# Optimization experiments

Hardware: AMD Instinct MI355X
Metric: run time of the kernel (lower is better)

The kernel has to match this reference:

```python
import jax, jax.numpy as jnp
import numpy as np

N_NODES = 500000
N_EDGES = 1250000
N_FEAT = 128
HIDDEN = 64
N_CLASSES = 10
N_GRAPHS = 512


def setup_inputs() -> dict:
    key = jax.random.key(0)
    ks = jax.random.split(key, 12)
    x = jax.random.normal(ks[0], (N_NODES, N_FEAT), dtype=jnp.float32)
    edge_index = jax.random.randint(ks[1], (2, N_EDGES), 0, N_NODES, dtype=jnp.int64)
    batch_index = jnp.sort(jax.random.randint(ks[2], (N_NODES,), 0, N_GRAPHS, dtype=jnp.int64))
    def glorot(k, fan_in, fan_out):
        s = jnp.sqrt(6.0 / (fan_in + fan_out))
        return jax.random.uniform(k, (fan_in, fan_out), jnp.float32, -s, s)
    return {
        "x": x,
        "edge_index": edge_index,
        "batch_index": batch_index,
        "W0": glorot(ks[3], N_FEAT, HIDDEN),
        "b0": jnp.zeros((HIDDEN,), jnp.float32),
        "W1": glorot(ks[4], HIDDEN, HIDDEN),
        "b1": jnp.zeros((HIDDEN,), jnp.float32),
        "W2": glorot(ks[5], HIDDEN, HIDDEN),
        "b2": jnp.zeros((HIDDEN,), jnp.float32),
        "Wout": glorot(ks[6], 2 * HIDDEN, N_CLASSES),
        "bout": jnp.zeros((N_CLASSES,), jnp.float32),
    }


def _gcn_norm(edge_index, n_nodes):
    # PyG GCNConv default: add self-loops, symmetric D^-1/2 (A+I) D^-1/2 norm.
    loop = jnp.arange(n_nodes, dtype=edge_index.dtype)
    src = jnp.concatenate([edge_index[0], loop])  # message sources
    dst = jnp.concatenate([edge_index[1], loop])  # aggregation targets
    deg = jax.ops.segment_sum(jnp.ones_like(dst, dtype=jnp.float32), dst,
                              num_segments=n_nodes)
    dinv = jnp.where(deg > 0, jax.lax.rsqrt(deg), 0.0)
    norm = dinv[src] * dinv[dst]  # [E+N]
    return src, dst, norm


def _gcn_conv(h, W, b, src, dst, norm, n_nodes):
    h = h @ W  # transform first (PyG applies lin before propagate)
    msg = h[src] * norm[:, None]  # gather + scale, [E+N, C]
    out = jax.ops.segment_sum(msg, dst, num_segments=n_nodes)
    return out + b


def reference(x, edge_index, batch_index, W0, b0, W1, b1, W2, b2, Wout, bout):
    n = x.shape[0]
    src, dst, norm = _gcn_norm(edge_index, n)
    h = jax.nn.relu(_gcn_conv(x, W0, b0, src, dst, norm, n))
    h = jax.nn.relu(_gcn_conv(h, W1, b1, src, dst, norm, n))
    h = jax.nn.relu(_gcn_conv(h, W2, b2, src, dst, norm, n))
    # global mean / max pool over graphs
    gsum = jax.ops.segment_sum(h, batch_index, num_segments=N_GRAPHS)
    cnt = jax.ops.segment_sum(jnp.ones((n,), jnp.float32), batch_index,
                              num_segments=N_GRAPHS)
    gmean = gsum / jnp.maximum(cnt, 1.0)[:, None]
    gmax = jax.ops.segment_max(h, batch_index, num_segments=N_GRAPHS)
    gmax = jnp.where(jnp.isneginf(gmax), 0.0, gmax)  # guard empty graphs
    pooled = jnp.concatenate([gmean, gmax], axis=1)  # [G, 2H]
    return pooled @ Wout + bout
```

## Files before the change

kernel.cpp:

```cpp
#include <hip/hip_runtime.h>
#include <hip/hip_bf16.h>

#define NN 500000
#define NE 1250000
#define NF 128
#define NH 64
#define NC 10
#define NG 512
#define ELLW 8

typedef __attribute__((ext_vector_type(8))) short short8;
typedef __attribute__((ext_vector_type(4))) float floatx4;

__device__ __forceinline__ unsigned short f2bf(float f) {
  unsigned u = __builtin_bit_cast(unsigned, f);
  u += 0x7FFFu + ((u >> 16) & 1u);
  return (unsigned short)(u >> 16);
}
__device__ __forceinline__ float bf2f(unsigned short u) {
  return __builtin_bit_cast(float, (unsigned)u << 16);
}
__device__ __forceinline__ float asf(int i) { return __builtin_bit_cast(float, i); }

__global__ __launch_bounds__(256) void k_init(int* __restrict__ deg, int* __restrict__ cur,
                                              int* __restrict__ counter,
                                              float* __restrict__ gsum, int* __restrict__ gmax,
                                              int* __restrict__ gcnt,
                                              int4* __restrict__ ell4,
                                              const float* __restrict__ W0,
                                              const float* __restrict__ W1,
                                              const float* __restrict__ W2,
                                              unsigned short* __restrict__ Wt0,
                                              unsigned short* __restrict__ Wt1,
                                              unsigned short* __restrict__ Wt2) {
  int i = blockIdx.x * 256 + threadIdx.x;
  if (i < NN) {
    deg[i] = 0; cur[i] = 0;
    int4 p; p.x = i; p.y = 0; p.z = i; p.w = 0;
    ell4[(size_t)i * 4 + 0] = p;
    ell4[(size_t)i * 4 + 1] = p;
    ell4[(size_t)i * 4 + 2] = p;
    ell4[(size_t)i * 4 + 3] = p;
  }
  if (i == 0) *counter = 0;
  if (i < NG * 64) { gsum[i] = 0.f; gmax[i] = 0; }
  if (i < NG) gcnt[i] = 0;
  if (i < NF * 64) { int k = i / 64, n = i % 64; Wt0[n * NF + k] = f2bf(W0[i]); }
  if (i < 64 * 64) {
    int k = i / 64, n = i % 64;
    Wt1[n * 64 + k] = f2bf(W1[i]);
    Wt2[n * 64 + k] = f2bf(W2[i]);
  }
}

__global__ __launch_bounds__(256) void k_deg(const int* __restrict__ dst, int* __restrict__ deg) {
  int e = blockIdx.x * 256 + threadIdx.x;
  if (e < NE) atomicAdd(&deg[dst[e]], 1);
}

__global__ __launch_bounds__(256) void k_dinv(const int* __restrict__ deg,
                                              float* __restrict__ dinv,
                                              int* __restrict__ odeg) {
  int i = blockIdx.x * 256 + threadIdx.x;
  if (i < NN) {
    int d = deg[i];
    dinv[i] = rsqrtf((float)(d + 1));
    odeg[i] = d > ELLW ? d - ELLW : 0;
  }
}

__global__ __launch_bounds__(256) void k_rowstart(const int* __restrict__ deg,
                                                  int* __restrict__ row_start,
                                                  int* __restrict__ counter) {
  int i = blockIdx.x * 256 + threadIdx.x;
  int lane = threadIdx.x & 63;
  int d = (i < NN) ? deg[i] : 0;
  int incl = d;
#pragma unroll
  for (int off = 1; off < 64; off <<= 1) {
    int n = __shfl_up(incl, off, 64);
    if (lane >= off) incl += n;
  }
  int total = __shfl(incl, 63, 64);
  int base = 0;
  if (lane == 63) base = atomicAdd(counter, total);
  base = __shfl(base, 63, 64);
  if (i < NN) row_start[i] = base + incl - d;
}

__global__ __launch_bounds__(256) void k_fill(const int* __restrict__ ei,
                                              const float* __restrict__ dinv,
                                              int* __restrict__ cur,
                                              int2* __restrict__ ell,
                                              const int* __restrict__ ostart,
                                              int2* __restrict__ ovf) {
  int e = blockIdx.x * 256 + threadIdx.x;
  if (e >= NE) return;
  int s = ei[e];
  int d = ei[NE + e];
  float nrm = dinv[s] * dinv[d];
  int slot = atomicAdd(&cur[d], 1);
  int2 v;
  v.x = s;
  v.y = __builtin_bit_cast(int, nrm);
  if (slot < ELLW) ell[(size_t)d * ELLW + slot] = v;
  else ovf[ostart[d] + slot - ELLW] = v;
}

__global__ __launch_bounds__(256) void k_gemm_f32(const float* __restrict__ Ain,
                                                  const unsigned short* __restrict__ Wt,
                                                  unsigned short* __restrict__ linbf) {
  constexpr int K = 128, KC = 4, SP = K + 8;
  __shared__ unsigned short Wl[64 * SP];
  int tid = threadIdx.x;
  for (int idx = tid * 8; idx < 64 * K; idx += 2048) {
    int n = idx / K, k = idx % K;
    *(short8*)&Wl[n * SP + k] = *(const short8*)&Wt[idx];
  }
  __syncthreads();

  int lane = tid & 63, wave = tid >> 6;
  int quad = lane >> 4, l16 = lane & 15;

  short8 bfrag[4][KC];
#pragma unroll
  for (int nt = 0; nt < 4; ++nt)
#pragma unroll
    for (int kc = 0; kc < KC; ++kc)
      bfrag[nt][kc] = *(const short8*)&Wl[(nt * 16 + l16) * SP + kc * 32 + quad * 8];

  const int ntiles = NN / 16;
  for (int t0 = (blockIdx.x * 4 + wave) * 2; t0 < ntiles; t0 += gridDim.x * 8) {
    floatx4 acc[2][4];
    floatx4 araw[2][KC][2];
#pragma unroll
    for (int tt = 0; tt < 2; ++tt) {
      int arow = (t0 + tt) * 16 + l16;
      const float* Ab = Ain + (size_t)arow * K + quad * 8;
#pragma unroll
      for (int kc = 0; kc < KC; ++kc) {
        araw[tt][kc][0] = *(const floatx4*)(Ab + kc * 32);
        araw[tt][kc][1] = *(const floatx4*)(Ab + kc * 32 + 4);
      }
    }
#pragma unroll
    for (int tt = 0; tt < 2; ++tt) {
      floatx4 z = {0.f, 0.f, 0.f, 0.f};
#pragma unroll
      for (int nt = 0; nt < 4; ++nt) acc[tt][nt] = z;
#pragma unroll
      for (int kc = 0; kc < KC; ++kc) {
        short8 af;
#pragma unroll
        for (int q = 0; q < 4; ++q) {
          af[q] = (short)f2bf(araw[tt][kc][0][q]);
          af[q + 4] = (short)f2bf(araw[tt][kc][1][q]);
        }
#pragma unroll
        for (int nt = 0; nt < 4; ++nt)
          acc[tt][nt] = __builtin_amdgcn_mfma_f32_16x16x32_bf16(af, bfrag[nt][kc], acc[tt][nt], 0, 0, 0);
      }
#pragma unroll
      for (int i = 0; i < 4; ++i) {
        int r = (t0 + tt) * 16 + quad * 4 + i;
        unsigned short* lp = linbf + (size_t)r * 64 + l16;
#pragma unroll
        for (int nt = 0; nt < 4; ++nt) lp[nt * 16] = f2bf(acc[tt][nt][i]);
      }
    }
  }
}

__global__ __launch_bounds__(256) void k_agg(const unsigned short* __restrict__ linbf,
                                             const float* __restrict__ dinv,
                                             const float* __restrict__ bias,
                                             const int* __restrict__ deg,
                                             const int2* __restrict__ ell,
                                             const int* __restrict__ ostart,
                                             const int2* __restrict__ ovf,
                                             unsigned short* __restrict__ hout) {
  int r = blockIdx.x * 4 + (threadIdx.x >> 6);
  if (r >= NN) return;
  int c = threadIdx.x & 63;
  const int4* ellv = (const int4*)(ell + (size_t)r * ELLW);
  int4 q0 = ellv[0], q1 = ellv[1], q2 = ellv[2], q3 = ellv[3];
  int dg = deg[r];
  float dv = dinv[r];
  float bc = bias[c];
  float acc = bf2f(linbf[(size_t)r * 64 + c]) * dv * dv;

  acc = fmaf(asf(q0.y), bf2f(linbf[(size_t)q0.x * 64 + c]), acc);
  acc = fmaf(asf(q0.w), bf2f(linbf[(size_t)q0.z * 64 + c]), acc);
  acc = fmaf(asf(q1.y), bf2f(linbf[(size_t)q1.x * 64 + c]), acc);
  acc = fmaf(asf(q1.w), bf2f(linbf[(size_t)q1.z * 64 + c]), acc);
  if (dg > 4) {
    acc = fmaf(asf(q2.y), bf2f(linbf[(size_t)q2.x * 64 + c]), acc);
    acc = fmaf(asf(q2.w), bf2f(linbf[(size_t)q2.z * 64 + c]), acc);
    acc = fmaf(asf(q3.y), bf2f(linbf[(size_t)q3.x * 64 + c]), acc);
    acc = fmaf(asf(q3.w), bf2f(linbf[(size_t)q3.z * 64 + c]), acc);
  }
  if (dg > ELLW) {
    int rs = ostart[r];
    int on = dg - ELLW;
    for (int j = 0; j < on; j += 4) {
      int2 e0 = ovf[rs + j];
      int2 e1 = ovf[rs + j + 1];
      int2 e2 = ovf[rs + j + 2];
      int2 e3 = ovf[rs + j + 3];
      int rem = on - j;
      float n0 = asf(e0.y);
      float n1 = rem > 1 ? asf(e1.y) : 0.f;
      float n2 = rem > 2 ? asf(e2.y) : 0.f;
      float n3 = rem > 3 ? asf(e3.y) : 0.f;
      int s0 = e0.x;
      int s1 = rem > 1 ? e1.x : r;
      int s2 = rem > 2 ? e2.x : r;
      int s3 = rem > 3 ? e3.x : r;
      acc = fmaf(n0, bf2f(linbf[(size_t)s0 * 64 + c]), acc);
      acc = fmaf(n1, bf2f(linbf[(size_t)s1 * 64 + c]), acc);
      acc = fmaf(n2, bf2f(linbf[(size_t)s2 * 64 + c]), acc);
      acc = fmaf(n3, bf2f(linbf[(size_t)s3 * 64 + c]), acc);
    }
  }
  hout[(size_t)r * 64 + c] = f2bf(fmaxf(acc + bc, 0.f));
}

template <int POOL>
__global__ __launch_bounds__(256) void k_layer(const unsigned short* __restrict__ hin,
                                               const float* __restrict__ dinv,
                                               const float* __restrict__ bias,
                                               const int* __restrict__ deg,
                                               const int2* __restrict__ ell,
                                               const int* __restrict__ ostart,
                                               const int2* __restrict__ ovf,
                                               const unsigned short* __restrict__ Wt,
                                               unsigned short* __restrict__ hout,
                                               float* __restrict__ gsum,
                                               int* __restrict__ gmax,
                                               int* __restrict__ gcnt,
                                               const int* __restrict__ batch) {
  constexpr int SP = 72;
  constexpr int SLDS = POOL ? (64 * 66 * 2) : (64 * SP);
  __shared__ unsigned short Sl[SLDS];
  float* smemf = (float*)Sl;
  int tid = threadIdx.x;
  int lane = tid & 63, wave = tid >> 6, quad = lane >> 4, l16 = lane & 15;

  for (int idx = tid * 8; idx < 64 * 64; idx += 2048)
    *(short8*)&Sl[idx] = *(const short8*)&Wt[idx];
  __syncthreads();
  short8 bfrag[4][2];
#pragma unroll
  for (int nt = 0; nt < 4; ++nt)
#pragma unroll
    for (int kc = 0; kc < 2; ++kc)
      bfrag[nt][kc] = *(const short8*)&Sl[(nt * 16 + l16) * 64 + kc * 32 + quad * 8];
  float bb[4];
#pragma unroll
  for (int nt = 0; nt < 4; ++nt) bb[nt] = bias[nt * 16 + l16];
  __syncthreads();

  int base = blockIdx.x * 64;
  int rbase = base + wave * 16;

#pragma unroll 4
  for (int j = 0; j < 16; ++j) {
    int r = rbase + j;
    float acc = 0.f;
    if (r < NN) {
      const int4* ellv = (const int4*)(ell + (size_t)r * ELLW);
      int4 q0 = ellv[0], q1 = ellv[1], q2 = ellv[2], q3 = ellv[3];
      int dg = deg[r];
      float dv = dinv[r];
      acc = bf2f(hin[(size_t)r * 64 + lane]) * dv * dv;
      acc = fmaf(asf(q0.y), bf2f(hin[(size_t)q0.x * 64 + lane]), acc);
      acc = fmaf(asf(q0.w), bf2f(hin[(size_t)q0.z * 64 + lane]), acc);
      acc = fmaf(asf(q1.y), bf2f(hin[(size_t)q1.x * 64 + lane]), acc);
      acc = fmaf(asf(q1.w), bf2f(hin[(size_t)q1.z * 64 + lane]), acc);
      if (dg > 4) {
        acc = fmaf(asf(q2.y), bf2f(hin[(size_t)q2.x * 64 + lane]), acc);
        acc = fmaf(asf(q2.w), bf2f(hin[(size_t)q2.z * 64 + lane]), acc);
        acc = fmaf(asf(q3.y), bf2f(hin[(size_t)q3.x * 64 + lane]), acc);
        acc = fmaf(asf(q3.w), bf2f(hin[(size_t)q3.z * 64 + lane]), acc);
      }
      if (dg > ELLW) {
        int rs = ostart[r];
        int on = dg - ELLW;
        for (int jj = 0; jj < on; jj += 4) {
          int2 e0 = ovf[rs + jj];
          int2 e1 = ovf[rs + jj + 1];
          int2 e2 = ovf[rs + jj + 2];
          int2 e3 = ovf[rs + jj + 3];
          int rem = on - jj;
          float n0 = asf(e0.y);
          float n1 = rem > 1 ? asf(e1.y) : 0.f;
          float n2 = rem > 2 ? asf(e2.y) : 0.f;
          float n3 = rem > 3 ? asf(e3.y) : 0.f;
          int s0 = e0.x;
          int s1 = rem > 1 ? e1.x : r;
          int s2 = rem > 2 ? e2.x : r;
          int s3 = rem > 3 ? e3.x : r;
          acc = fmaf(n0, bf2f(hin[(size_t)s0 * 64 + lane]), acc);
          acc = fmaf(n1, bf2f(hin[(size_t)s1 * 64 + lane]), acc);
          acc = fmaf(n2, bf2f(hin[(size_t)s2 * 64 + lane]), acc);
          acc = fmaf(n3, bf2f(hin[(size_t)s3 * 64 + lane]), acc);
        }
      }
    }
    Sl[(wave * 16 + j) * SP + lane] = f2bf(acc);
  }

  floatx4 z = {0.f, 0.f, 0.f, 0.f};
  floatx4 acc4[4] = {z, z, z, z};
#pragma unroll
  for (int kc = 0; kc < 2; ++kc) {
    short8 af = *(const short8*)&Sl[(wave * 16 + l16) * SP + kc * 32 + quad * 8];
#pragma unroll
    for (int nt = 0; nt < 4; ++nt)
      acc4[nt] = __builtin_amdgcn_mfma_f32_16x16x32_bf16(af, bfrag[nt][kc], acc4[nt], 0, 0, 0);
  }

  if constexpr (!POOL) {
#pragma unroll
    for (int i = 0; i < 4; ++i) {
      int r = rbase + quad * 4 + i;
      if (r < NN) {
        unsigned short* hp = hout + (size_t)r * 64 + l16;
#pragma unroll
        for (int nt = 0; nt < 4; ++nt)
          hp[nt * 16] = f2bf(fmaxf(acc4[nt][i] + bb[nt], 0.f));
      }
    }
  } else {
    __shared__ int sb[64];
    __shared__ float reds[256];
    __shared__ float redm[256];
    __shared__ int redc[4];
    __syncthreads();
#pragma unroll
    for (int i = 0; i < 4; ++i) {
      int row = wave * 16 + quad * 4 + i;
#pragma unroll
      for (int nt = 0; nt < 4; ++nt)
        smemf[row * 66 + nt * 16 + l16] = fmaxf(acc4[nt][i] + bb[nt], 0.f);
    }
    if (tid < 64) sb[tid] = (base + tid < NN) ? batch[base + tid] : 0x7fffffff;
    __syncthreads();
    int nvalid = NN - base; if (nvalid > 64) nvalid = 64;
    int gs = sb[0], ge = sb[nvalid - 1];
    int feat = tid & 63, strip = tid >> 6;
    for (int g = gs; g <= ge; ++g) {
      float s = 0.f, m = 0.f;
      int cl = 0;
#pragma unroll
      for (int j = 0; j < 16; ++j) {
        int row = strip * 16 + j;
        float v = smemf[row * 66 + feat];
        if (sb[row] == g) { s += v; m = fmaxf(m, v); cl++; }
      }
      reds[tid] = s;
      redm[tid] = m;
      if (feat == 0) redc[strip] = cl;
      __syncthreads();
      if (strip == 0) {
        s += reds[64 + feat] + reds[128 + feat] + reds[192 + feat];
        m = fmaxf(fmaxf(m, redm[64 + feat]), fmaxf(redm[128 + feat], redm[192 + feat]));
        atomicAdd(&gsum[g * 64 + feat], s);
        atomicMax(&gmax[g * 64 + feat], __builtin_bit_cast(int, m));
        if (feat == 0) atomicAdd(&gcnt[g], redc[0] + redc[1] + redc[2] + redc[3]);
      }
      __syncthreads();
    }
  }
}

__global__ __launch_bounds__(128) void k_head(const float* __restrict__ gsum,
                                              const int* __restrict__ gmax,
                                              const int* __restrict__ gcnt,
                                              const float* __restrict__ Wout,
                                              const float* __restrict__ bout,
                                              float* __restrict__ out) {
  __shared__ float p[128];
  int g = blockIdx.x, tid = threadIdx.x;
  if (tid < 64) {
    int c = gcnt[g];
    float inv = c > 0 ? 1.0f / (float)c : 0.f;
    p[tid] = gsum[g * 64 + tid] * inv;
    p[64 + tid] = asf(gmax[g * 64 + tid]);
  }
  __syncthreads();
  if (tid < NC) {
    float acc = bout[tid];
#pragma unroll 8
    for (int c2 = 0; c2 < 128; ++c2) acc += p[c2] * Wout[c2 * NC + tid];
    out[g * NC + tid] = acc;
  }
}

extern "C" void kernel_launch(void* const* d_in, const int* in_sizes, int n_in,
                              void* d_out, int out_size, void* d_ws, size_t ws_size,
                              hipStream_t stream) {
  const float* x     = (const float*)d_in[0];
  const int*   ei    = (const int*)d_in[1];
  const int*   batch = (const int*)d_in[2];
  const float* W0    = (const float*)d_in[3];
  const float* b0    = (const float*)d_in[4];
  const float* W1    = (const float*)d_in[5];
  const float* b1    = (const float*)d_in[6];
  const float* W2    = (const float*)d_in[7];
  const float* b2    = (const float*)d_in[8];
  const float* Wout  = (const float*)d_in[9];
  const float* bout  = (const float*)d_in[10];
  float* out = (float*)d_out;

  char* ws = (char*)d_ws;
  size_t off = 0;
  auto alloc = [&](size_t bytes) -> void* {
    void* p = ws + off;
    off = (off + bytes + 255) & ~(size_t)255;
    return p;
  };
  int*   deg     = (int*)alloc((size_t)NN * 4);
  int*   odeg    = (int*)alloc((size_t)NN * 4);
  int*   counter = (int*)alloc(4);
  float* dinv    = (float*)alloc((size_t)NN * 4);
  int*   ostart  = (int*)alloc((size_t)NN * 4);
  int*   cur     = (int*)alloc((size_t)NN * 4);
  int2*  ell     = (int2*)alloc((size_t)NN * ELLW * 8);
  int2*  ovf     = (int2*)alloc(((size_t)NE + 4) * 8);
  unsigned short* linbf = (unsigned short*)alloc((size_t)NN * 64 * 2);
  unsigned short* H1    = (unsigned short*)alloc((size_t)NN * 64 * 2);
  unsigned short* H2    = (unsigned short*)alloc((size_t)NN * 64 * 2);
  unsigned short* Wt0 = (unsigned short*)alloc(64 * 128 * 2);
  unsigned short* Wt1 = (unsigned short*)alloc(64 * 64 * 2);
  unsigned short* Wt2 = (unsigned short*)alloc(64 * 64 * 2);
  float* gsum = (float*)alloc((size_t)NG * 64 * 4);
  int*   gmax = (int*)alloc((size_t)NG * 64 * 4);
  int*   gcnt = (int*)alloc((size_t)NG * 4);

  k_init<<<(NN + 255) / 256, 256, 0, stream>>>(deg, cur, counter, gsum, gmax, gcnt,
                                               (int4*)ell, W0, W1, W2, Wt0, Wt1, Wt2);
  k_deg<<<(NE + 255) / 256, 256, 0, stream>>>(ei + NE, deg);
  k_dinv<<<(NN + 255) / 256, 256, 0, stream>>>(deg, dinv, odeg);
  k_rowstart<<<(NN + 255) / 256, 256, 0, stream>>>(odeg, ostart, counter);
  k_fill<<<(NE + 255) / 256, 256, 0, stream>>>(ei, dinv, cur, ell, ostart, ovf);

  k_gemm_f32<<<2048, 256, 0, stream>>>(x, Wt0, linbf);
  k_agg<<<(NN + 3) / 4, 256, 0, stream>>>(linbf, dinv, b0, deg, ell, ostart, ovf, H1);
  k_layer<0><<<(NN + 63) / 64, 256, 0, stream>>>(H1, dinv, b1, deg, ell, ostart, ovf, Wt1, H2,
                                                 nullptr, nullptr, nullptr, nullptr);
  k_layer<1><<<(NN + 63) / 64, 256, 0, stream>>>(H2, dinv, b2, deg, ell, ostart, ovf, Wt2, nullptr,
                                                 gsum, gmax, gcnt, batch);
  k_head<<<NG, 128, 0, stream>>>(gsum, gmax, gcnt, Wout, bout, out);
}
```

Measured before the change: 958.3 us.

## Vectorize neighbor gathers with 8-lane-per-row short8 loads and fuse dinv/rowstart

The aggregation in k_agg and k_layer now assigns 8 lanes per node, each loading a 16-byte short8 of features, so a wave processes 8 rows in parallel instead of one. This replaces scalar 2-byte gathers with wide loads and gives more independent memory requests in flight. The weights move to their own LDS buffer so the aggregation can run before the first barrier. Separately, k_dinv and k_rowstart are merged into a single kernel, dropping the odeg buffer and one launch. The overflow loop is unrolled by 2 instead of 4, and k_agg assumes NN is a multiple of 32.

```diff
diff --git a/kernel.cpp b/kernel.cpp
--- a/kernel.cpp
+++ b/kernel.cpp
@@ -21,6 +21,11 @@
   return __builtin_bit_cast(float, (unsigned)u << 16);
 }
 __device__ __forceinline__ float asf(int i) { return __builtin_bit_cast(float, i); }
+
+__device__ __forceinline__ void fma8(float acc[8], float n, short8 v) {
+#pragma unroll
+  for (int k = 0; k < 8; ++k) acc[k] = fmaf(n, bf2f((unsigned short)v[k]), acc[k]);
+}
 
 __global__ __launch_bounds__(256) void k_init(int* __restrict__ deg, int* __restrict__ cur,
                                               int* __restrict__ counter,
@@ -58,24 +63,19 @@
   if (e < NE) atomicAdd(&deg[dst[e]], 1);
 }
 
-__global__ __launch_bounds__(256) void k_dinv(const int* __restrict__ deg,
-                                              float* __restrict__ dinv,
-                                              int* __restrict__ odeg) {
-  int i = blockIdx.x * 256 + threadIdx.x;
-  if (i < NN) {
-    int d = deg[i];
-    dinv[i] = rsqrtf((float)(d + 1));
-    odeg[i] = d > ELLW ? d - ELLW : 0;
-  }
-}
-
-__global__ __launch_bounds__(256) void k_rowstart(const int* __restrict__ deg,
-                                                  int* __restrict__ row_start,
-                                                  int* __restrict__ counter) {
+__global__ __launch_bounds__(256) void k_dinv_rs(const int* __restrict__ deg,
+                                                 float* __restrict__ dinv,
+                                                 int* __restrict__ row_start,
+                                                 int* __restrict__ counter) {
   int i = blockIdx.x * 256 + threadIdx.x;
   int lane = threadIdx.x & 63;
-  int d = (i < NN) ? deg[i] : 0;
-  int incl = d;
+  int d = 0;
+  if (i < NN) {
+    d = deg[i];
+    dinv[i] = rsqrtf((float)(d + 1));
+  }
+  int od = d > ELLW ? d - ELLW : 0;
+  int incl = od;
 #pragma unroll
   for (int off = 1; off < 64; off <<= 1) {
     int n = __shfl_up(incl, off, 64);
@@ -85,7 +85,7 @@
   int base = 0;
   if (lane == 63) base = atomicAdd(counter, total);
   base = __shfl(base, 63, 64);
-  if (i < NN) row_start[i] = base + incl - d;
+  if (i < NN) row_start[i] = base + incl - od;
 }
 
 __global__ __launch_bounds__(256) void k_fill(const int* __restrict__ ei,
@@ -179,50 +179,61 @@
                                              const int* __restrict__ ostart,
                                              const int2* __restrict__ ovf,
                                              unsigned short* __restrict__ hout) {
-  int r = blockIdx.x * 4 + (threadIdx.x >> 6);
-  if (r >= NN) return;
-  int c = threadIdx.x & 63;
+  int tid = threadIdx.x;
+  int lane = tid & 63, wave = tid >> 6;
+  int g = lane >> 3, sl = lane & 7, fb = sl * 8;
+  int r = blockIdx.x * 32 + wave * 8 + g;
+
   const int4* ellv = (const int4*)(ell + (size_t)r * ELLW);
   int4 q0 = ellv[0], q1 = ellv[1], q2 = ellv[2], q3 = ellv[3];
   int dg = deg[r];
   float dv = dinv[r];
-  float bc = bias[c];
-  float acc = bf2f(linbf[(size_t)r * 64 + c]) * dv * dv;
-
-  acc = fmaf(asf(q0.y), bf2f(linbf[(size_t)q0.x * 64 + c]), acc);
-  acc = fmaf(asf(q0.w), bf2f(linbf[(size_t)q0.z * 64 + c]), acc);
-  acc = fmaf(asf(q1.y), bf2f(linbf[(size_t)q1.x * 64 + c]), acc);
-  acc = fmaf(asf(q1.w), bf2f(linbf[(size_t)q1.z * 64 + c]), acc);
+  short8 hs = *(const short8*)&linbf[(size_t)r * 64 + fb];
+  short8 g0 = *(const short8*)&linbf[(size_t)q0.x * 64 + fb];
+  short8 g1 = *(const short8*)&linbf[(size_t)q0.z * 64 + fb];
+  short8 g2 = *(const short8*)&linbf[(size_t)q1.x * 64 + fb];
+  short8 g3 = *(const short8*)&linbf[(size_t)q1.z * 64 + fb];
+  float acc[8];
+  float sw = dv * dv;
+#pragma unroll
+  for (int k = 0; k < 8; ++k) acc[k] = bf2f((unsigned short)hs[k]) * sw;
+  fma8(acc, asf(q0.y), g0);
+  fma8(acc, asf(q0.w), g1);
+  fma8(acc, asf(q1.y), g2);
+  fma8(acc, asf(q1.w), g3);
   if (dg > 4) {
-    acc = fmaf(asf(q2.y), bf2f(linbf[(size_t)q2.x * 64 + c]), acc);
-    acc = fmaf(asf(q2.w), bf2f(linbf[(size_t)q2.z * 64 + c]), acc);
-    acc = fmaf(asf(q3.y), bf2f(linbf[(size_t)q3.x * 64 + c]), acc);
-    acc = fmaf(asf(q3.w), bf2f(linbf[(size_t)q3.z * 64 + c]), acc);
+    short8 g4 = *(const short8*)&linbf[(size_t)q2.x * 64 + fb];
+    short8 g5 = *(const short8*)&linbf[(size_t)q2.z * 64 + fb];
+    short8 g6 = *(const short8*)&linbf[(size_t)q3.x * 64 + fb];
+    short8 g7 = *(const short8*)&linbf[(size_t)q3.z * 64 + fb];
+    fma8(acc, asf(q2.y), g4);
+    fma8(acc, asf(q2.w), g5);
+    fma8(acc, asf(q3.y), g6);
+    fma8(acc, asf(q3.w), g7);
   }
   if (dg > ELLW) {
-    int rs = ostart[r];
-    int on = dg - ELLW;
-    for (int j = 0; j < on; j += 4) {
+    int rs = ostart[r], on = dg - ELLW;
+    for (int j = 0; j < on; j += 2) {
       int2 e0 = ovf[rs + j];
       int2 e1 = ovf[rs + j + 1];
-      int2 e2 = ovf[rs + j + 2];
-      int2 e3 = ovf[rs + j + 3];
       int rem = on - j;
-      float n0 = asf(e0.y);
+      int sx1 = rem > 1 ? e1.x : r;
       float n1 = rem > 1 ? asf(e1.y) : 0.f;
-      float n2 = rem > 2 ? asf(e2.y) : 0.f;
-      float n3 = rem > 3 ? asf(e3.y) : 0.f;
-      int s0 = e0.x;
-      int s1 = rem > 1 ? e1.x : r;
-      int s2 = rem > 2 ? e2.x : r;
-      int s3 = rem > 3 ? e3.x : r;
-      acc = fmaf(n0, bf2f(linbf[(size_t)s0 * 64 + c]), acc);
-      acc = fmaf(n1, bf2f(linbf[(size_t)s1 * 64 + c]), acc);
-      acc = fmaf(n2, bf2f(linbf[(size_t)s2 * 64 + c]), acc);
-      acc = fmaf(n3, bf2f(linbf[(size_t)s3 * 64 + c]), acc);
-    }
-  }
-  hout[(size_t)r * 64 + c] = f2bf(fmaxf(acc + bc, 0.f));
+      short8 f0 = *(const short8*)&linbf[(size_t)e0.x * 64 + fb];
+      short8 f1 = *(const short8*)&linbf[(size_t)sx1 * 64 + fb];
+      fma8(acc, asf(e0.y), f0);
+      fma8(acc, n1, f1);
+    }
+  }
+  floatx4 bv0 = *(const floatx4*)&bias[fb];
+  floatx4 bv1 = *(const floatx4*)&bias[fb + 4];
+  short8 o;
+#pragma unroll
+  for (int k = 0; k < 8; ++k) {
+    float bk = k < 4 ? bv0[k] : bv1[k - 4];
+    o[k] = (short)f2bf(fmaxf(acc[k] + bk, 0.f));
+  }
+  *(short8*)&hout[(size_t)r * 64 + fb] = o;
 }
 
 template <int POOL>
@@ -241,74 +252,82 @@
                                                const int* __restrict__ batch) {
   constexpr int SP = 72;
   constexpr int SLDS = POOL ? (64 * 66 * 2) : (64 * SP);
+  __shared__ unsigned short Wl[64 * 64];
   __shared__ unsigned short Sl[SLDS];
   float* smemf = (float*)Sl;
   int tid = threadIdx.x;
   int lane = tid & 63, wave = tid >> 6, quad = lane >> 4, l16 = lane & 15;
+  int g = lane >> 3, sl = lane & 7, fb = sl * 8;
 
   for (int idx = tid * 8; idx < 64 * 64; idx += 2048)
-    *(short8*)&Sl[idx] = *(const short8*)&Wt[idx];
+    *(short8*)&Wl[idx] = *(const short8*)&Wt[idx];
+
+  float bb[4];
+#pragma unroll
+  for (int nt = 0; nt < 4; ++nt) bb[nt] = bias[nt * 16 + l16];
+
+  int base = blockIdx.x * 64;
+
+#pragma unroll
+  for (int it = 0; it < 2; ++it) {
+    int row = wave * 16 + it * 8 + g;
+    int r = base + row;
+    int rr = r < NN ? r : NN - 1;
+    const int4* ellv = (const int4*)(ell + (size_t)rr * ELLW);
+    int4 q0 = ellv[0], q1 = ellv[1], q2 = ellv[2], q3 = ellv[3];
+    int dg = deg[rr];
+    float dv = dinv[rr];
+    short8 hs = *(const short8*)&hin[(size_t)rr * 64 + fb];
+    short8 g0 = *(const short8*)&hin[(size_t)q0.x * 64 + fb];
+    short8 g1 = *(const short8*)&hin[(size_t)q0.z * 64 + fb];
+    short8 g2 = *(const short8*)&hin[(size_t)q1.x * 64 + fb];
+    short8 g3 = *(const short8*)&hin[(size_t)q1.z * 64 + fb];
+    float acc[8];
+    float sw = dv * dv;
+#pragma unroll
+    for (int k = 0; k < 8; ++k) acc[k] = bf2f((unsigned short)hs[k]) * sw;
+    fma8(acc, asf(q0.y), g0);
+    fma8(acc, asf(q0.w), g1);
+    fma8(acc, asf(q1.y), g2);
+    fma8(acc, asf(q1.w), g3);
+    if (dg > 4) {
+      short8 g4 = *(const short8*)&hin[(size_t)q2.x * 64 + fb];
+      short8 g5 = *(const short8*)&hin[(size_t)q2.z * 64 + fb];
+      short8 g6 = *(const short8*)&hin[(size_t)q3.x * 64 + fb];
+      short8 g7 = *(const short8*)&hin[(size_t)q3.z * 64 + fb];
+      fma8(acc, asf(q2.y), g4);
+      fma8(acc, asf(q2.w), g5);
+      fma8(acc, asf(q3.y), g6);
+      fma8(acc, asf(q3.w), g7);
+    }
+    if (dg > ELLW) {
+      int rs = ostart[rr], on = dg - ELLW;
+      for (int j = 0; j < on; j += 2) {
+        int2 e0 = ovf[rs + j];
+        int2 e1 = ovf[rs + j + 1];
+        int rem = on - j;
+        int sx1 = rem > 1 ? e1.x : rr;
+        float n1 = rem > 1 ? asf(e1.y) : 0.f;
+        short8 f0 = *(const short8*)&hin[(size_t)e0.x * 64 + fb];
+        short8 f1 = *(const short8*)&hin[(size_t)sx1 * 64 + fb];
+        fma8(acc, asf(e0.y), f0);
+        fma8(acc, n1, f1);
+      }
+    }
+    short8 o;
+#pragma unroll
+    for (int k = 0; k < 8; ++k) o[k] = (short)f2bf(acc[k]);
+    *(short8*)&Sl[row * SP + fb] = o;
+  }
+
   __syncthreads();
+
   short8 bfrag[4][2];
 #pragma unroll
   for (int nt = 0; nt < 4; ++nt)
 #pragma unroll
     for (int kc = 0; kc < 2; ++kc)
-      bfrag[nt][kc] = *(const short8*)&Sl[(nt * 16 + l16) * 64 + kc * 32 + quad * 8];
-  float bb[4];
-#pragma unroll
-  for (int nt = 0; nt < 4; ++nt) bb[nt] = bias[nt * 16 + l16];
-  __syncthreads();
-
-  int base = blockIdx.x * 64;
-  int rbase = base + wave * 16;
-
-#pragma unroll 4
-  for (int j = 0; j < 16; ++j) {
-    int r = rbase + j;
-    float acc = 0.f;
-    if (r < NN) {
-      const int4* ellv = (const int4*)(ell + (size_t)r * ELLW);
-      int4 q0 = ellv[0], q1 = ellv[1], q2 = ellv[2], q3 = ellv[3];
-      int dg = deg[r];
-      float dv = dinv[r];
-      acc = bf2f(hin[(size_t)r * 64 + lane]) * dv * dv;
-      acc = fmaf(asf(q0.y), bf2f(hin[(size_t)q0.x * 64 + lane]), acc);
-      acc = fmaf(asf(q0.w), bf2f(hin[(size_t)q0.z * 64 + lane]), acc);
-      acc = fmaf(asf(q1.y), bf2f(hin[(size_t)q1.x * 64 + lane]), acc);
-      acc = fmaf(asf(q1.w), bf2f(hin[(size_t)q1.z * 64 + lane]), acc);
-      if (dg > 4) {
-        acc = fmaf(asf(q2.y), bf2f(hin[(size_t)q2.x * 64 + lane]), acc);
-        acc = fmaf(asf(q2.w), bf2f(hin[(size_t)q2.z * 64 + lane]), acc);
-        acc = fmaf(asf(q3.y), bf2f(hin[(size_t)q3.x * 64 + lane]), acc);
-        acc = fmaf(asf(q3.w), bf2f(hin[(size_t)q3.z * 64 + lane]), acc);
-      }
-      if (dg > ELLW) {
-        int rs = ostart[r];
-        int on = dg - ELLW;
-        for (int jj = 0; jj < on; jj += 4) {
-          int2 e0 = ovf[rs + jj];
-          int2 e1 = ovf[rs + jj + 1];
-          int2 e2 = ovf[rs + jj + 2];
-          int2 e3 = ovf[rs + jj + 3];
-          int rem = on - jj;
-          float n0 = asf(e0.y);
-          float n1 = rem > 1 ? asf(e1.y) : 0.f;
-          float n2 = rem > 2 ? asf(e2.y) : 0.f;
-          float n3 = rem > 3 ? asf(e3.y) : 0.f;
-          int s0 = e0.x;
-          int s1 = rem > 1 ? e1.x : r;
-          int s2 = rem > 2 ? e2.x : r;
-          int s3 = rem > 3 ? e3.x : r;
-          acc = fmaf(n0, bf2f(hin[(size_t)s0 * 64 + lane]), acc);
-          acc = fmaf(n1, bf2f(hin[(size_t)s1 * 64 + lane]), acc);
-          acc = fmaf(n2, bf2f(hin[(size_t)s2 * 64 + lane]), acc);
-          acc = fmaf(n3, bf2f(hin[(size_t)s3 * 64 + lane]), acc);
-        }
-      }
-    }
-    Sl[(wave * 16 + j) * SP + lane] = f2bf(acc);
-  }
+      bfrag[nt][kc] = *(const short8*)&Wl[(nt * 16 + l16) * 64 + kc * 32 + quad * 8];
 
   floatx4 z = {0.f, 0.f, 0.f, 0.f};
   floatx4 acc4[4] = {z, z, z, z};
@@ -323,7 +342,7 @@
   if constexpr (!POOL) {
 #pragma unroll
     for (int i = 0; i < 4; ++i) {
-      int r = rbase + quad * 4 + i;
+      int r = base + wave * 16 + quad * 4 + i;
       if (r < NN) {
         unsigned short* hp = hout + (size_t)r * 64 + l16;
 #pragma unroll
@@ -349,14 +368,14 @@
     int nvalid = NN - base; if (nvalid > 64) nvalid = 64;
     int gs = sb[0], ge = sb[nvalid - 1];
     int feat = tid & 63, strip = tid >> 6;
-    for (int g = gs; g <= ge; ++g) {
+    for (int gg = gs; gg <= ge; ++gg) {
       float s = 0.f, m = 0.f;
       int cl = 0;
 #pragma unroll
       for (int j = 0; j < 16; ++j) {
         int row = strip * 16 + j;
         float v = smemf[row * 66 + feat];
-        if (sb[row] == g) { s += v; m = fmaxf(m, v); cl++; }
+        if (sb[row] == gg) { s += v; m = fmaxf(m, v); cl++; }
       }
       reds[tid] = s;
       redm[tid] = m;
@@ -365,9 +384,9 @@
       if (strip == 0) {
         s += reds[64 + feat] + reds[128 + feat] + reds[192 + feat];
         m = fmaxf(fmaxf(m, redm[64 + feat]), fmaxf(redm[128 + feat], redm[192 + feat]));
-        atomicAdd(&gsum[g * 64 + feat], s);
-        atomicMax(&gmax[g * 64 + feat], __builtin_bit_cast(int, m));
-        if (feat == 0) atomicAdd(&gcnt[g], redc[0] + redc[1] + redc[2] + redc[3]);
+        atomicAdd(&gsum[gg * 64 + feat], s);
+        atomicMax(&gmax[gg * 64 + feat], __builtin_bit_cast(int, m));
+        if (feat == 0) atomicAdd(&gcnt[gg], redc[0] + redc[1] + redc[2] + redc[3]);
       }
       __syncthreads();
     }
@@ -421,7 +440,6 @@
     return p;
   };
   int*   deg     = (int*)alloc((size_t)NN * 4);
-  int*   odeg    = (int*)alloc((size_t)NN * 4);
   int*   counter = (int*)alloc(4);
   float* dinv    = (float*)alloc((size_t)NN * 4);
   int*   ostart  = (int*)alloc((size_t)NN * 4);
@@ -441,12 +459,11 @@
   k_init<<<(NN + 255) / 256, 256, 0, stream>>>(deg, cur, counter, gsum, gmax, gcnt,
                                                (int4*)ell, W0, W1, W2, Wt0, Wt1, Wt2);
   k_deg<<<(NE + 255) / 256, 256, 0, stream>>>(ei + NE, deg);
-  k_dinv<<<(NN + 255) / 256, 256, 0, stream>>>(deg, dinv, odeg);
-  k_rowstart<<<(NN + 255) / 256, 256, 0, stream>>>(odeg, ostart, counter);
+  k_dinv_rs<<<(NN + 255) / 256, 256, 0, stream>>>(deg, dinv, ostart, counter);
   k_fill<<<(NE + 255) / 256, 256, 0, stream>>>(ei, dinv, cur, ell, ostart, ovf);
 
   k_gemm_f32<<<2048, 256, 0, stream>>>(x, Wt0, linbf);
-  k_agg<<<(NN + 3) / 4, 256, 0, stream>>>(linbf, dinv, b0, deg, ell, ostart, ovf, H1);
+  k_agg<<<NN / 32, 256, 0, stream>>>(linbf, dinv, b0, deg, ell, ostart, ovf, H1);
   k_layer<0><<<(NN + 63) / 64, 256, 0, stream>>>(H1, dinv, b1, deg, ell, ostart, ovf, Wt1, H2,
                                                  nullptr, nullptr, nullptr, nullptr);
   k_layer<1><<<(NN + 63) / 64, 256, 0, stream>>>(H2, dinv, b2, deg, ell, ostart, ovf, Wt2, nullptr,
```

New measurement: 775.9 us. -19.0%, faster.
